# Kernel optimization log

Measured on AMD Instinct MI355X. Metric: run time of the kernel, lower is better.

The kernel has to match this reference:

```python
import jax, jax.numpy as jnp
import numpy as np
import math

IN_CH = 256; ORDER = 8; K = 9; B = 32; L = 8192


def _conv1d(x, w, b, dilation, padding):
    # x: [B,C,L], w: [O,C,k]
    y = jax.lax.conv_general_dilated(x, w, (1,), [(padding, padding)],
                                     rhs_dilation=(dilation,),
                                     dimension_numbers=('NCH', 'OIH', 'NCH'))
    return y + b[None, :, None]


def _bn(x, g, beta, eps=1e-5):
    # training-mode BatchNorm1d: batch statistics over (B, L), biased variance
    m = x.mean(axis=(0, 2), keepdims=True)
    v = ((x - m) ** 2).mean(axis=(0, 2), keepdims=True)
    return g[None, :, None] * (x - m) * jax.lax.rsqrt(v + eps) + beta[None, :, None]


def _adaptive_r(x, p):
    # p = (c1w,c1b,c2w,c2b,g1,b1,g2,b2,g3,b3,pxw,pxb,fcw,fcb)
    a = jax.nn.relu(_bn(_conv1d(x, p[0], p[1], 1, 1), p[4], p[5]))
    b2 = jax.nn.relu(_bn(_conv1d(x, p[2], p[3], 2, 2), p[6], p[7]))
    c = jax.nn.relu(_bn(_conv1d(a + b2, p[10], p[11], 1, 0), p[8], p[9]))
    pooled = c.mean(axis=2)                      # AdaptiveAvgPool1d(1) + flatten
    return pooled @ p[12].T + p[13]              # [B,1]


def _hermite_kernel(t):
    # t: [B,K] -> kernel [B, ORDER, K]
    hs = [jnp.ones_like(t), 2.0 * t]
    for i in range(2, ORDER - 1):
        hs.append(2.0 * t * hs[-1] - 2.0 * (i - 1) * hs[-2])
    exp_term = jnp.exp(-0.5 * t * t)
    fs = []
    for i in range(ORDER - 1):
        const = 2.0 ** (i / 2) / math.sqrt(math.pi * math.factorial(i))
        f = exp_term * (const * hs[i])
        norm = jnp.linalg.norm(f, axis=1, keepdims=True)
        fs.append(f / jnp.clip(norm, 1e-12))
    fs.append(jax.nn.sigmoid(2.0 * t))           # 1/(1+exp(-2t))
    return jnp.stack(fs, axis=1)


def _forward(x, conv1_w, conv1_b, conv2_b, wp, cp):
    # conv1 is kernel-size-1 -> pointwise GEMM
    x1 = jnp.einsum('bil,oi->bol', x, conv1_w[:, :, 0]) + conv1_b[None, :, None]
    width = _adaptive_r(x1, wp)                  # [B,1]
    center = jnp.clip(_adaptive_r(x1, cp), 1.0, 128.0)
    T = jnp.arange(K, dtype=x.dtype)[None, :]
    t = width * (T - center)                     # [B,K]
    kernel = _hermite_kernel(t)                  # [B,ORDER,K]
    # batched per-sample conv1d (the torch loop over B) as one einsum pass
    pad = K // 2
    Lx = x1.shape[2]
    x1p = jnp.pad(x1, ((0, 0), (0, 0), (pad, pad)))
    out = sum(jnp.einsum('bcl,bc->bl', x1p[:, :, j:j + Lx], kernel[:, :, j])
              for j in range(K))
    out = out[:, None, :] + conv2_b[None, :, None]   # [B,1,L]
    return out, x1


def setup_inputs() -> dict:
    key = jax.random.key(0)
    ks = iter(jax.random.split(key, 64))
    def rn(shape, s=0.05):
        return jax.random.normal(next(ks), shape, dtype=jnp.float32) * s
    d = {
        'x': jax.random.normal(next(ks), (B, IN_CH, L), dtype=jnp.float32),
        'conv1_w': rn((ORDER, IN_CH, 1)),
        'conv1_b': jnp.zeros((ORDER,), jnp.float32),
        'conv2_b': jnp.zeros((1,), jnp.float32),
    }
    for pre in ('w_', 'c_'):
        d[pre + 'c1w'] = rn((ORDER, ORDER, 3)); d[pre + 'c1b'] = jnp.zeros((ORDER,), jnp.float32)
        d[pre + 'c2w'] = rn((ORDER, ORDER, 3)); d[pre + 'c2b'] = jnp.zeros((ORDER,), jnp.float32)
        for g in ('g1', 'g2', 'g3'):
            d[pre + g] = jnp.ones((ORDER,), jnp.float32)
        for bn in ('b1', 'b2', 'b3'):
            d[pre + bn] = jnp.zeros((ORDER,), jnp.float32)
        d[pre + 'pxw'] = rn((ORDER, ORDER, 1)); d[pre + 'pxb'] = jnp.zeros((ORDER,), jnp.float32)
        d[pre + 'fcw'] = rn((1, ORDER), 0.1); d[pre + 'fcb'] = jnp.zeros((1,), jnp.float32)
    return d


def reference(x, conv1_w, conv1_b, conv2_b,
              w_c1w, w_c1b, w_c2w, w_c2b, w_g1, w_b1, w_g2, w_b2, w_g3, w_b3,
              w_pxw, w_pxb, w_fcw, w_fcb,
              c_c1w, c_c1b, c_c2w, c_c2b, c_g1, c_b1, c_g2, c_b2, c_g3, c_b3,
              c_pxw, c_pxb, c_fcw, c_fcb):
    wp = (w_c1w, w_c1b, w_c2w, w_c2b, w_g1, w_b1, w_g2, w_b2, w_g3, w_b3,
          w_pxw, w_pxb, w_fcw, w_fcb)
    cp = (c_c1w, c_c1b, c_c2w, c_c2b, c_g1, c_b1, c_g2, c_b2, c_g3, c_b3,
          c_pxw, c_pxb, c_fcw, c_fcb)
    return _forward(x, conv1_w, conv1_b, conv2_b, wp, cp)
```

## Files before the change

### kernel.cpp

```cpp
#include <hip/hip_runtime.h>
#include <math.h>

#define BATCH 32
#define CIN   256
#define LEN   8192
#define HL    (LEN/2)
#define ORD   8
#define NPOS  (BATCH*LEN)

struct Params { const float* p[32]; };


__device__ __forceinline__ void wave_reduce2(float& sv, float& sq)
{
#pragma unroll
    for (int m = 32; m >= 1; m >>= 1) {
        sv += __shfl_xor(sv, m, 64);
        sq += __shfl_xor(sq, m, 64);
    }
}
__device__ __forceinline__ void wave_reduce1(float& sv)
{
#pragma unroll
    for (int m = 32; m >= 1; m >>= 1) sv += __shfl_xor(sv, m, 64);
}

__device__ __forceinline__ void load_conv_lds(const Params& P, float* wl, float* bl, int tid)
{
    for (int idx = tid; idx < 4*192; idx += 256) {
        int which = idx / 192, s = idx - which*192;
        const float* src = (which==0) ? P.p[4] : (which==1) ? P.p[6]
                         : (which==2) ? P.p[18] : P.p[20];
        wl[idx] = src[s];
    }
    if (tid < 32) {
        int wq = tid >> 3, o = tid & 7;
        const float* bsrc = (wq==0) ? P.p[5] : (wq==1) ? P.p[7]
                          : (wq==2) ? P.p[19] : P.p[21];
        bl[tid] = bsrc[o];
    }
}

__device__ __forceinline__ void conv6_pair_lds(
    const float xv[8][6], const float* wl, float bv, int dil, int row,
    float& r0, float& r1)
{
    float a0 = bv, a1 = bv;
    const float4* wr4 = reinterpret_cast<const float4*>(wl + row*24);
    float wr[24];
#pragma unroll
    for (int q = 0; q < 6; q++) *reinterpret_cast<float4*>(&wr[4*q]) = wr4[q];
#pragma unroll
    for (int i = 0; i < 8; i++) {
        float w0 = wr[i*3+0], w1 = wr[i*3+1], w2 = wr[i*3+2];
        if (dil == 1) {
            a0 += w0*xv[i][1] + w1*xv[i][2] + w2*xv[i][3];
            a1 += w0*xv[i][2] + w1*xv[i][3] + w2*xv[i][4];
        } else {
            a0 += w0*xv[i][0] + w1*xv[i][2] + w2*xv[i][4];
            a1 += w0*xv[i][1] + w1*xv[i][3] + w2*xv[i][5];
        }
    }
    r0 = a0; r1 = a1;
}

#define XT_W 264
#define LOAD_XV6(xt, tp, xv)                                  \
    _Pragma("unroll")                                         \
    for (int i_ = 0; i_ < 8; i_++) {                          \
        _Pragma("unroll")                                     \
        for (int d_ = 0; d_ < 6; d_++)                        \
            xv[i_][d_] = xt[i_][2 + 2*(tp) + d_];             \
    }

__device__ __forceinline__ void stage_tile256(
    const float* __restrict__ x1, int b, int t0, float (*xt)[XT_W], int tid)
{
    int ch = tid >> 5, q = tid & 31;
    const float* src = x1 + ((size_t)b*ORD + ch)*LEN + t0;
    float4 a0 = *reinterpret_cast<const float4*>(src + q*8);
    float4 a1 = *reinterpret_cast<const float4*>(src + q*8 + 4);
    *reinterpret_cast<float4*>(&xt[ch][4 + q*8]) = a0;
    *reinterpret_cast<float4*>(&xt[ch][8 + q*8]) = a1;
    if (tid < 32) {
        int hc = tid >> 2, hh = tid & 3;
        int l   = t0 + ((hh < 2) ? (hh - 2) : (254 + hh));
        int idx = (hh < 2) ? (2 + hh) : (258 + hh);
        xt[hc][idx] = ((unsigned)l < (unsigned)LEN)
                    ? x1[((size_t)b*ORD + hc)*LEN + l] : 0.f;
    }
}

__global__ __launch_bounds__(256, 4) void k1_gemm_stats(
    const float* __restrict__ x, const float* __restrict__ w,
    const float* __restrict__ bias, float* __restrict__ x1,
    float* __restrict__ ws, Params P)
{
    __shared__ float wt[CIN][ORD];
    __shared__ float xt[ORD][XT_W];
    __shared__ float hbuf[4][257];
    __shared__ float wl[768], bl[32];
    __shared__ float part[128];
    int tid = threadIdx.x;
    for (int idx = tid; idx < CIN*ORD; idx += 256) {
        int o = idx >> 8, i = idx & 255;
        wt[i][o] = w[idx];
    }
    load_conv_lds(P, wl, bl, tid);

    int b  = blockIdx.x >> 5;
    int t0 = (blockIdx.x & 31) << 8;

    const float* xch = x + ((size_t)b*CIN + tid)*LEN;
    float h0 = 0.f, h1 = 0.f, h2 = 0.f, h3 = 0.f;
    if (t0 >= 2)        { h0 = xch[t0-2];   h1 = xch[t0-1]; }
    if (t0 + 257 < LEN) { h2 = xch[t0+256]; h3 = xch[t0+257]; }
    __syncthreads();

    const int ihalf = tid >> 7;
    const int pos2  = tid & 127;
    const float2* xrow = reinterpret_cast<const float2*>(x)
                       + (size_t)b*CIN*HL + (size_t)ihalf*128*HL
                       + (t0 >> 1) + pos2;
    float2 acc[ORD];
#pragma unroll
    for (int o = 0; o < ORD; o++) { acc[o].x = 0.f; acc[o].y = 0.f; }

#pragma unroll 8
    for (int ii = 0; ii < 128; ii++) {
        float2 xv2 = xrow[(size_t)ii * HL];
        const float4* wr = reinterpret_cast<const float4*>(&wt[ihalf*128 + ii][0]);
        float4 wa = wr[0], wb = wr[1];
        acc[0].x += xv2.x*wa.x; acc[0].y += xv2.y*wa.x;
        acc[1].x += xv2.x*wa.y; acc[1].y += xv2.y*wa.y;
        acc[2].x += xv2.x*wa.z; acc[2].y += xv2.y*wa.z;
        acc[3].x += xv2.x*wa.w; acc[3].y += xv2.y*wa.w;
        acc[4].x += xv2.x*wb.x; acc[4].y += xv2.y*wb.x;
        acc[5].x += xv2.x*wb.y; acc[5].y += xv2.y*wb.y;
        acc[6].x += xv2.x*wb.z; acc[6].y += xv2.y*wb.z;
        acc[7].x += xv2.x*wb.w; acc[7].y += xv2.y*wb.w;
    }

    if (ihalf == 1) {
#pragma unroll
        for (int o = 0; o < ORD; o++)
            *reinterpret_cast<float2*>(&xt[o][4 + 2*pos2]) = acc[o];
    }
    hbuf[0][tid] = h0; hbuf[1][tid] = h1; hbuf[2][tid] = h2; hbuf[3][tid] = h3;
    __syncthreads();
    if (ihalf == 0) {
        float2* x1row = reinterpret_cast<float2*>(x1)
                      + (size_t)b*ORD*HL + (t0 >> 1) + pos2;
#pragma unroll
        for (int o = 0; o < ORD; o++) {
            float2 v = *reinterpret_cast<const float2*>(&xt[o][4 + 2*pos2]);
            float bo = bias[o];
            float2 r; r.x = acc[o].x + v.x + bo; r.y = acc[o].y + v.y + bo;
            *reinterpret_cast<float2*>(&xt[o][4 + 2*pos2]) = r;
            x1row[(size_t)o * HL] = r;
        }
    }
    if (tid < 32) {
        int hq = tid >> 3, ch = tid & 7;
        int l  = t0 + ((hq < 2) ? (hq - 2) : (254 + hq));
        float a = 0.f;
        if ((unsigned)l < (unsigned)LEN) {
            a = bias[ch];
#pragma unroll 8
            for (int i = 0; i < CIN; i++) a += hbuf[hq][i] * wt[i][ch];
        }
        int idx = (hq < 2) ? (2 + hq) : (258 + hq);
        xt[ch][idx] = a;
    }
    __syncthreads();

    const int tp = tid & 127;
    float xv[8][6];
    LOAD_XV6(xt, tp, xv);

    int lane = tid & 63, wv = tid >> 6;
    int gbase = (wv >> 1) * 2;
#pragma unroll
    for (int gg = 0; gg < 2; gg++) {
        int grp = gbase + gg;
#pragma unroll
        for (int o = 0; o < 8; o++) {
            int c = grp*8 + o;
            float a0, a1;
            if (gg == 0) conv6_pair_lds(xv, wl, bl[c], 1, c, a0, a1);
            else         conv6_pair_lds(xv, wl, bl[c], 2, c, a0, a1);
            float sv = a0 + a1, sq = a0*a0 + a1*a1;
            wave_reduce2(sv, sq);
            if (lane == 0) {
                part[c*2 + (wv&1)]        = sv;
                part[(32 + c)*2 + (wv&1)] = sq;
            }
        }
    }
    __syncthreads();
    if (tid < 64) {
        float s = part[tid*2] + part[tid*2+1];
        atomicAdd(&ws[tid], s);
    }
}

__global__ __launch_bounds__(256, 4) void k3_cpre_stats(
    const float* __restrict__ x1, float* __restrict__ ws,
    float* __restrict__ cpre, Params P)
{
    __shared__ float wl[768], bl[32];
    __shared__ float pxl[128], pxbl[16];
    __shared__ float scl[32], shf[32];
    __shared__ float xt[ORD][XT_W];
    __shared__ float part[64];
    int tid = threadIdx.x;
    load_conv_lds(P, wl, bl, tid);
    if (tid >= 128) { int q = tid - 128; pxl[q] = (q < 64) ? P.p[14][q] : P.p[28][q-64]; }
    if (tid >= 112 && tid < 128) { int q = tid - 112; pxbl[q] = (q < 8) ? P.p[15][q] : P.p[29][q-8]; }
    if (tid >= 32 && tid < 64) {
        int c = tid - 32;
        int br = c >> 4, cv = (c >> 3) & 1, o = c & 7;
        const float Ninv = 1.0f / (float)NPOS;
        float m   = ws[c]      * Ninv;
        float var = ws[32 + c] * Ninv - m*m;
        const float* g  = P.p[ br ? (cv?23:22) : (cv?9:8)  ];
        const float* be = P.p[ br ? (cv?26:25) : (cv?12:11)];
        float sc = g[o] * rsqrtf(var + 1e-5f);
        scl[c] = sc; shf[c] = be[o] - m*sc;
    }
    int b  = blockIdx.x >> 5;
    int t0 = (blockIdx.x & 31) << 8;
    stage_tile256(x1, b, t0, xt, tid);
    __syncthreads();

    const int tp = tid & 127;
    const int br = tid >> 7;
    float xv[8][6];
    LOAD_XV6(xt, tp, xv);

    int lane = tid & 63, wv = tid >> 6;
    float s0[8], s1[8];
#pragma unroll
    for (int ch = 0; ch < 8; ch++) {
        int ca = (br*2+0)*8 + ch, cb = (br*2+1)*8 + ch;
        float a0, a1, c0, c1;
        conv6_pair_lds(xv, wl, bl[ca], 1, ca, a0, a1);
        conv6_pair_lds(xv, wl, bl[cb], 2, cb, c0, c1);
        s0[ch] = fmaxf(a0*scl[ca] + shf[ca], 0.f) + fmaxf(c0*scl[cb] + shf[cb], 0.f);
        s1[ch] = fmaxf(a1*scl[ca] + shf[ca], 0.f) + fmaxf(c1*scl[cb] + shf[cb], 0.f);
    }
#pragma unroll
    for (int o = 0; o < 8; o++) {
        float a0 = pxbl[br*8 + o], a1 = a0;
#pragma unroll
        for (int i = 0; i < 8; i++) {
            a0 += pxl[br*64 + o*8 + i] * s0[i];
            a1 += pxl[br*64 + o*8 + i] * s1[i];
        }
        int c = br*8 + o;
        float2 st; st.x = a0; st.y = a1;
        *reinterpret_cast<float2*>(
            &cpre[(size_t)c*NPOS + (size_t)b*LEN + t0 + 2*tp]) = st;
        float sv = a0 + a1, sq = a0*a0 + a1*a1;
        wave_reduce2(sv, sq);
        if (lane == 0) {
            part[c*2 + (wv&1)]        = sv;
            part[32 + c*2 + (wv&1)]   = sq;
        }
    }
    __syncthreads();
    if (tid < 32) {
        float s = part[tid*2] + part[tid*2+1];
        atomicAdd(&ws[64 + tid], s);
    }
}

__global__ __launch_bounds__(256) void k4_light(
    const float* __restrict__ cpre, float* __restrict__ ws, Params P)
{
    __shared__ float scl3[16], shf3[16];
    __shared__ float part[64];
    int tid = threadIdx.x;
    const float Ninv = 1.0f / (float)NPOS;
    if (tid < 16) {
        int br = tid >> 3, o = tid & 7;
        float m3 = ws[64 + tid] * Ninv;
        float v3 = ws[80 + tid] * Ninv - m3*m3;
        const float* g3 = P.p[ br ? 24 : 10 ];
        const float* b3 = P.p[ br ? 27 : 13 ];
        float sc = g3[o] * rsqrtf(v3 + 1e-5f);
        scl3[tid] = sc; shf3[tid] = b3[o] - m3*sc;
    }
    __syncthreads();

    int b  = blockIdx.x >> 4;
    int t0 = (blockIdx.x & 15) << 9;
    int lane = tid & 63, wv = tid >> 6;
#pragma unroll
    for (int c = 0; c < 16; c++) {
        float2 v = *reinterpret_cast<const float2*>(
            &cpre[(size_t)c*NPOS + (size_t)b*LEN + t0 + 2*tid]);
        float sv = fmaxf(v.x*scl3[c] + shf3[c], 0.f)
                 + fmaxf(v.y*scl3[c] + shf3[c], 0.f);
        wave_reduce1(sv);
        if (lane == 0) part[c*4 + wv] = sv;
    }
    __syncthreads();
    if (tid < 16) {
        float s = part[tid*4] + part[tid*4+1] + part[tid*4+2] + part[tid*4+3];
        atomicAdd(&ws[96 + (tid >> 3)*256 + b*8 + (tid & 7)], s);
    }
}

#define XT6_W 272
__global__ __launch_bounds__(256) void k6_out(
    const float* __restrict__ x1, const float* __restrict__ ws, Params P,
    float* __restrict__ out)
{
    __shared__ float kern[8][9];
    __shared__ float xt[8][XT6_W];
    int tid = threadIdx.x;
    int b  = blockIdx.x >> 5;
    int t0 = (blockIdx.x & 31) << 8;

    {
        int ch = tid >> 5, q = tid & 31;
        const float* src = x1 + ((size_t)b*ORD + ch)*LEN + t0;
        float4 a0 = *reinterpret_cast<const float4*>(src + q*8);
        float4 a1 = *reinterpret_cast<const float4*>(src + q*8 + 4);
        *reinterpret_cast<float4*>(&xt[ch][8  + q*8]) = a0;
        *reinterpret_cast<float4*>(&xt[ch][12 + q*8]) = a1;
        if (q < 4) {
            int l = t0 - 4 + q;
            xt[ch][4 + q] = (l >= 0) ? src[q - 4] : 0.f;
        } else if (q < 8) {
            int l = t0 + 256 + (q - 4);
            xt[ch][260 + q] = (l < LEN) ? src[256 + q - 4] : 0.f;
        }
    }

    if (tid < 9) {
        const float Li = 1.0f / (float)LEN;
        float vw = P.p[17][0], vc = P.p[31][0];
#pragma unroll
        for (int ch = 0; ch < 8; ch++) {
            vw += P.p[16][ch] * (ws[96 +       b*8 + ch] * Li);
            vc += P.p[30][ch] * (ws[96 + 256 + b*8 + ch] * Li);
        }
        float width  = vw;
        float center = fminf(fmaxf(vc, 1.0f), 128.0f);

        float cst[7];
        cst[0] = 0.56418958354775628f;
#pragma unroll
        for (int i = 1; i < 7; i++) cst[i] = cst[i-1] * sqrtf(2.0f / (float)i);

        int k = tid;
        float t = width * ((float)k - center);
        float e = expf(-0.5f * t * t);
        float hp = 1.0f, hc = 2.0f * t;
        kern[0][k] = e * cst[0];
        kern[1][k] = e * cst[1] * hc;
#pragma unroll
        for (int i = 2; i < 7; i++) {
            float hn = 2.0f*t*hc - 2.0f*(float)(i-1)*hp;
            hp = hc; hc = hn;
            kern[i][k] = e * cst[i] * hc;
        }
        kern[7][k] = 1.0f / (1.0f + expf(-2.0f * t));
    }
    __syncthreads();
    if (tid < 7) {
        float ss = 0.f;
#pragma unroll
        for (int k = 0; k < 9; k++) ss += kern[tid][k]*kern[tid][k];
        float inv = 1.0f / fmaxf(sqrtf(ss), 1e-12f);
#pragma unroll
        for (int k = 0; k < 9; k++) kern[tid][k] *= inv;
    }
    __syncthreads();

    float acc = P.p[3][0];
#pragma unroll
    for (int c = 0; c < 8; c++) {
#pragma unroll
        for (int j = 0; j < 9; j++) acc += xt[c][4 + tid + j] * kern[c][j];
    }
    out[(size_t)b*LEN + t0 + tid] = acc;
}

extern "C" void kernel_launch(void* const* d_in, const int* in_sizes, int n_in,
                              void* d_out, int out_size, void* d_ws, size_t ws_size,
                              hipStream_t stream)
{
    (void)in_sizes; (void)n_in; (void)out_size; (void)ws_size;
    const float* x  = (const float*)d_in[0];
    const float* w1 = (const float*)d_in[1];
    const float* b1 = (const float*)d_in[2];
    float* outF = (float*)d_out;
    float* x1   = outF + (size_t)BATCH * LEN;
    float* ws   = (float*)d_ws;
    float* cpre = ws + 1024;

    Params P;
    for (int i = 0; i < 32; i++) P.p[i] = (const float*)d_in[i];

    hipMemsetAsync(d_ws, 0, 4096, stream);
    k1_gemm_stats<<<1024, 256, 0, stream>>>(x, w1, b1, x1, ws, P);
    k3_cpre_stats<<<1024, 256, 0, stream>>>(x1, ws, cpre, P);
    k4_light     <<<512,  256, 0, stream>>>(cpre, ws, P);
    k6_out       <<<1024, 256, 0, stream>>>(x1, ws, P, outF);
}
```

Before: 142.6 us.

## Enlarge k1 tiles to 1024 positions with 1024-thread blocks

The GEMM+stats kernel now processes 1024 sequence positions per block with 1024 threads, one position per thread over all 256 input channels, instead of 256 positions split over two channel halves. This removes the cross-half LDS reduction and extra sync, and cuts per-block overhead (weight staging, halo loads, halo GEMM) relative to the work done. The stats conv runs on 512 threads, each computing two outputs, with 8 partial sums per channel. It risks lower occupancy from the larger shared memory and block size, and only 256 blocks are launched.

```diff
diff --git a/kernel.cpp b/kernel.cpp
--- a/kernel.cpp
+++ b/kernel.cpp
@@ -91,115 +91,109 @@
     }
 }
 
-__global__ __launch_bounds__(256, 4) void k1_gemm_stats(
+#define XT1_W 1036
+__global__ __launch_bounds__(1024, 4) void k1_gemm_stats(
     const float* __restrict__ x, const float* __restrict__ w,
     const float* __restrict__ bias, float* __restrict__ x1,
     float* __restrict__ ws, Params P)
 {
     __shared__ float wt[CIN][ORD];
-    __shared__ float xt[ORD][XT_W];
+    __shared__ float xt[ORD][XT1_W];
     __shared__ float hbuf[4][257];
     __shared__ float wl[768], bl[32];
-    __shared__ float part[128];
+    __shared__ float part[512];
     int tid = threadIdx.x;
-    for (int idx = tid; idx < CIN*ORD; idx += 256) {
+    for (int idx = tid; idx < CIN*ORD; idx += 1024) {
         int o = idx >> 8, i = idx & 255;
         wt[i][o] = w[idx];
     }
-    load_conv_lds(P, wl, bl, tid);
-
-    int b  = blockIdx.x >> 5;
-    int t0 = (blockIdx.x & 31) << 8;
-
-    const float* xch = x + ((size_t)b*CIN + tid)*LEN;
+    if (tid < 768) {
+        int which = tid / 192, s = tid - which*192;
+        const float* src = (which==0) ? P.p[4] : (which==1) ? P.p[6]
+                         : (which==2) ? P.p[18] : P.p[20];
+        wl[tid] = src[s];
+    }
+    if (tid >= 768 && tid < 800) {
+        int q = tid - 768, wq = q >> 3, o = q & 7;
+        const float* bsrc = (wq==0) ? P.p[5] : (wq==1) ? P.p[7]
+                          : (wq==2) ? P.p[19] : P.p[21];
+        bl[q] = bsrc[o];
+    }
+
+    int b  = blockIdx.x >> 3;
+    int t0 = (blockIdx.x & 7) << 10;
+
     float h0 = 0.f, h1 = 0.f, h2 = 0.f, h3 = 0.f;
-    if (t0 >= 2)        { h0 = xch[t0-2];   h1 = xch[t0-1]; }
-    if (t0 + 257 < LEN) { h2 = xch[t0+256]; h3 = xch[t0+257]; }
-    __syncthreads();
-
-    const int ihalf = tid >> 7;
-    const int pos2  = tid & 127;
-    const float2* xrow = reinterpret_cast<const float2*>(x)
-                       + (size_t)b*CIN*HL + (size_t)ihalf*128*HL
-                       + (t0 >> 1) + pos2;
-    float2 acc[ORD];
-#pragma unroll
-    for (int o = 0; o < ORD; o++) { acc[o].x = 0.f; acc[o].y = 0.f; }
+    if (tid < 256) {
+        const float* xch = x + ((size_t)b*CIN + tid)*LEN;
+        if (t0 >= 2)         { h0 = xch[t0-2];    h1 = xch[t0-1]; }
+        if (t0 + 1025 < LEN) { h2 = xch[t0+1024]; h3 = xch[t0+1025]; }
+    }
+    __syncthreads();
+
+    const float* xrow = x + (size_t)b*CIN*LEN + t0 + tid;
+    float acc[ORD];
+#pragma unroll
+    for (int o = 0; o < ORD; o++) acc[o] = 0.f;
 
 #pragma unroll 8
-    for (int ii = 0; ii < 128; ii++) {
-        float2 xv2 = xrow[(size_t)ii * HL];
-        const float4* wr = reinterpret_cast<const float4*>(&wt[ihalf*128 + ii][0]);
+    for (int i = 0; i < CIN; i++) {
+        float xv = xrow[(size_t)i * LEN];
+        const float4* wr = reinterpret_cast<const float4*>(&wt[i][0]);
         float4 wa = wr[0], wb = wr[1];
-        acc[0].x += xv2.x*wa.x; acc[0].y += xv2.y*wa.x;
-        acc[1].x += xv2.x*wa.y; acc[1].y += xv2.y*wa.y;
-        acc[2].x += xv2.x*wa.z; acc[2].y += xv2.y*wa.z;
-        acc[3].x += xv2.x*wa.w; acc[3].y += xv2.y*wa.w;
-        acc[4].x += xv2.x*wb.x; acc[4].y += xv2.y*wb.x;
-        acc[5].x += xv2.x*wb.y; acc[5].y += xv2.y*wb.y;
-        acc[6].x += xv2.x*wb.z; acc[6].y += xv2.y*wb.z;
-        acc[7].x += xv2.x*wb.w; acc[7].y += xv2.y*wb.w;
-    }
-
-    if (ihalf == 1) {
-#pragma unroll
-        for (int o = 0; o < ORD; o++)
-            *reinterpret_cast<float2*>(&xt[o][4 + 2*pos2]) = acc[o];
-    }
-    hbuf[0][tid] = h0; hbuf[1][tid] = h1; hbuf[2][tid] = h2; hbuf[3][tid] = h3;
-    __syncthreads();
-    if (ihalf == 0) {
-        float2* x1row = reinterpret_cast<float2*>(x1)
-                      + (size_t)b*ORD*HL + (t0 >> 1) + pos2;
-#pragma unroll
-        for (int o = 0; o < ORD; o++) {
-            float2 v = *reinterpret_cast<const float2*>(&xt[o][4 + 2*pos2]);
-            float bo = bias[o];
-            float2 r; r.x = acc[o].x + v.x + bo; r.y = acc[o].y + v.y + bo;
-            *reinterpret_cast<float2*>(&xt[o][4 + 2*pos2]) = r;
-            x1row[(size_t)o * HL] = r;
-        }
-    }
+        acc[0] += xv*wa.x; acc[1] += xv*wa.y; acc[2] += xv*wa.z; acc[3] += xv*wa.w;
+        acc[4] += xv*wb.x; acc[5] += xv*wb.y; acc[6] += xv*wb.z; acc[7] += xv*wb.w;
+    }
+
+    float* x1b = x1 + (size_t)b*ORD*LEN + t0 + tid;
+#pragma unroll
+    for (int o = 0; o < ORD; o++) {
+        float r = acc[o] + bias[o];
+        x1b[(size_t)o * LEN] = r;
+        xt[o][4 + tid] = r;
+    }
+    if (tid < 256) {
+        hbuf[0][tid] = h0; hbuf[1][tid] = h1; hbuf[2][tid] = h2; hbuf[3][tid] = h3;
+    }
+    __syncthreads();
+
     if (tid < 32) {
         int hq = tid >> 3, ch = tid & 7;
-        int l  = t0 + ((hq < 2) ? (hq - 2) : (254 + hq));
+        int l  = t0 + ((hq < 2) ? (hq - 2) : (1022 + hq));
         float a = 0.f;
         if ((unsigned)l < (unsigned)LEN) {
             a = bias[ch];
 #pragma unroll 8
             for (int i = 0; i < CIN; i++) a += hbuf[hq][i] * wt[i][ch];
         }
-        int idx = (hq < 2) ? (2 + hq) : (258 + hq);
+        int idx = (hq < 2) ? (2 + hq) : (1026 + hq);
         xt[ch][idx] = a;
     }
     __syncthreads();
 
-    const int tp = tid & 127;
-    float xv[8][6];
-    LOAD_XV6(xt, tp, xv);
-
-    int lane = tid & 63, wv = tid >> 6;
-    int gbase = (wv >> 1) * 2;
-#pragma unroll
-    for (int gg = 0; gg < 2; gg++) {
-        int grp = gbase + gg;
-#pragma unroll
-        for (int o = 0; o < 8; o++) {
-            int c = grp*8 + o;
-            float a0, a1;
-            if (gg == 0) conv6_pair_lds(xv, wl, bl[c], 1, c, a0, a1);
-            else         conv6_pair_lds(xv, wl, bl[c], 2, c, a0, a1);
-            float sv = a0 + a1, sq = a0*a0 + a1*a1;
-            wave_reduce2(sv, sq);
-            if (lane == 0) {
-                part[c*2 + (wv&1)]        = sv;
-                part[(32 + c)*2 + (wv&1)] = sq;
+    if (tid < 512) {
+        int tp = tid;
+        float xv[8][6];
+        LOAD_XV6(xt, tp, xv);
+        int lane = tid & 63, wv = tid >> 6;
+#pragma unroll
+        for (int grp = 0; grp < 4; grp++) {
+#pragma unroll
+            for (int o = 0; o < 8; o++) {
+                int c = grp*8 + o;
+                float a0, a1;
+                if (grp & 1) conv6_pair_lds(xv, wl, bl[c], 2, c, a0, a1);
+                else         conv6_pair_lds(xv, wl, bl[c], 1, c, a0, a1);
+                float sv = a0 + a1, sq = a0*a0 + a1*a1;
+                wave_reduce2(sv, sq);
+                if (lane == 0) { part[c*8 + wv] = sv; part[256 + c*8 + wv] = sq; }
             }
         }
     }
     __syncthreads();
     if (tid < 64) {
-        float s = part[tid*2] + part[tid*2+1];
+        const float* pp = &part[(tid < 32) ? tid*8 : 256 + (tid-32)*8];
+        float s = pp[0]+pp[1]+pp[2]+pp[3]+pp[4]+pp[5]+pp[6]+pp[7];
         atomicAdd(&ws[tid], s);
     }
 }
@@ -406,8 +400,8 @@
     for (int i = 0; i < 32; i++) P.p[i] = (const float*)d_in[i];
 
     hipMemsetAsync(d_ws, 0, 4096, stream);
-    k1_gemm_stats<<<1024, 256, 0, stream>>>(x, w1, b1, x1, ws, P);
-    k3_cpre_stats<<<1024, 256, 0, stream>>>(x1, ws, cpre, P);
-    k4_light     <<<512,  256, 0, stream>>>(cpre, ws, P);
-    k6_out       <<<1024, 256, 0, stream>>>(x1, ws, P, outF);
-}
+    k1_gemm_stats<<<256,  1024, 0, stream>>>(x, w1, b1, x1, ws, P);
+    k3_cpre_stats<<<1024, 256,  0, stream>>>(x1, ws, cpre, P);
+    k4_light     <<<512,  256,  0, stream>>>(cpre, ws, P);
+    k6_out       <<<1024, 256,  0, stream>>>(x1, ws, P, outF);
+}
```

Result: faster. 126.0 us (-11.6%).
